# Optimization experiments

Hardware: AMD Instinct MI355X
Metric: run time of the kernel (lower is better)

The kernel has to match this reference:

```python
import jax, jax.numpy as jnp
import numpy as np

B, C, Himg, Wimg = 32, 256, 64, 64
P = 8            # partition (window) size
HEADS, DH = 8, 32
SEQ = P * P      # tokens per window = 64
SCALE = C ** (-0.5)  # note: feat_dim**-0.5, as in the source
EPS = 1e-5


def _relative_position_index(h, w):
    coords = np.stack(np.meshgrid(np.arange(h), np.arange(w), indexing='ij'))  # [2,h,w]
    cf = coords.reshape(2, -1)
    rel = cf[:, :, None] - cf[:, None, :]            # [2,hw,hw]
    rel = rel.transpose(1, 2, 0)
    rel[:, :, 0] += h - 1
    rel[:, :, 1] += w - 1
    rel[:, :, 0] *= 2 * w - 1
    return rel.sum(-1)                               # [hw,hw] int

REL_IDX = jnp.asarray(_relative_position_index(P, P).reshape(-1))  # [SEQ*SEQ]


def layernorm(x, g, b):
    mu = jnp.mean(x, -1, keepdims=True)
    var = jnp.mean(jnp.square(x - mu), -1, keepdims=True)
    return (x - mu) * jax.lax.rsqrt(var + EPS) * g + b


def setup_inputs() -> dict:
    key = jax.random.key(0)
    ks = jax.random.split(key, 12)
    d = {}
    d['x'] = jax.random.normal(ks[0], (B, C, Himg, Wimg), jnp.float32)
    d['ln1_g'] = jnp.ones((C,), jnp.float32)
    d['ln1_b'] = jnp.zeros((C,), jnp.float32)
    d['qkv_w'] = jax.random.normal(ks[1], (C, 3 * C), jnp.float32) * 0.02
    d['qkv_b'] = jnp.zeros((3 * C,), jnp.float32)
    d['merge_w'] = jax.random.normal(ks[2], (C, C), jnp.float32) * 0.02
    d['merge_b'] = jnp.zeros((C,), jnp.float32)
    d['bias_table'] = jax.random.normal(ks[3], ((2 * P - 1) * (2 * P - 1), HEADS), jnp.float32) * 0.02
    d['ln2_g'] = jnp.ones((C,), jnp.float32)
    d['ln2_b'] = jnp.zeros((C,), jnp.float32)
    d['mlp_w1'] = jax.random.normal(ks[4], (C, 4 * C), jnp.float32) * 0.02
    d['mlp_b1'] = jnp.zeros((4 * C,), jnp.float32)
    d['mlp_w2'] = jax.random.normal(ks[5], (4 * C, C), jnp.float32) * 0.02
    d['mlp_b2'] = jnp.zeros((C,), jnp.float32)
    return d


def reference(x, ln1_g, ln1_b, qkv_w, qkv_b, merge_w, merge_b, bias_table,
              ln2_g, ln2_b, mlp_w1, mlp_b1, mlp_w2, mlp_b2):
    Bn, Cn, H, W = x.shape
    hp, wp = H // P, W // P
    # window partition: [B,C,H,W] -> [B, G, P*P, C]
    xw = x.reshape(Bn, Cn, hp, P, wp, P).transpose(0, 2, 4, 3, 5, 1)
    xw = xw.reshape(Bn, hp * wp, P * P, Cn)

    # --- attention block ---
    h = layernorm(xw, ln1_g, ln1_b)
    qkv = h @ qkv_w + qkv_b                                    # [B,G,S,3C]
    q, k, v = jnp.split(qkv, 3, axis=-1)
    def heads(t):
        return t.reshape(Bn, hp * wp, SEQ, HEADS, DH).transpose(0, 1, 3, 2, 4)
    q, k, v = heads(q), heads(k) * SCALE, heads(v)             # [B,G,h,S,d]
    scores = jnp.einsum('bghid,bghjd->bghij', q, k)            # [B,G,h,S,S]
    rel_bias = bias_table[REL_IDX].reshape(SEQ, SEQ, HEADS).transpose(2, 0, 1)
    attn = jax.nn.softmax(scores + rel_bias[None, None], axis=-1)
    out = jnp.einsum('bghij,bghjd->bghid', attn, v)            # [B,G,h,S,d]
    out = out.transpose(0, 1, 3, 2, 4).reshape(Bn, hp * wp, SEQ, Cn)
    xw = xw + (out @ merge_w + merge_b)

    # --- MLP block ---
    h = layernorm(xw, ln2_g, ln2_b)
    h = jax.nn.gelu(h @ mlp_w1 + mlp_b1, approximate=False)
    xw = xw + (h @ mlp_w2 + mlp_b2)

    # window departition: [B,G,P*P,C] -> [B,C,H,W]
    y = xw.reshape(Bn, hp, wp, P, P, Cn).transpose(0, 5, 1, 3, 2, 4)
    return y.reshape(Bn, Cn, hp * P, wp * P)
```

## Files before the change

kernel.cpp:

```cpp
#include <hip/hip_runtime.h>

typedef __attribute__((ext_vector_type(8))) short short8;
typedef __attribute__((ext_vector_type(4))) short short4v;
typedef __attribute__((ext_vector_type(8))) unsigned short ushort8v;
typedef __attribute__((ext_vector_type(4))) float f32x4;
typedef __attribute__((ext_vector_type(4))) int int4v;
typedef __attribute__((ext_vector_type(4))) unsigned short ushort4v;
typedef __attribute__((ext_vector_type(2))) unsigned short ushort2v;

#define SCALE_F 0.0625f
#define EPS_F 1e-5f

__device__ __forceinline__ float bf2f(unsigned short u) {
  unsigned int i = ((unsigned int)u) << 16;
  return __builtin_bit_cast(float, i);
}
__device__ __forceinline__ unsigned short f2bf(float f) {
  unsigned int i = __builtin_bit_cast(unsigned int, f);
  i += 0x7fffu + ((i >> 16) & 1u);
  return (unsigned short)(i >> 16);
}

__device__ __forceinline__ float fast_gelu(float v) {
  float s = v * v;
  float u = v * __builtin_fmaf(s, 0.0713548163f, 1.5957691216f);
  float e = __expf(u);
  float r = __builtin_amdgcn_rcpf(e + 1.f);
  return v - v * r;
}

__device__ __forceinline__ void gload_lds16(const unsigned short* g, unsigned short* l) {
  __builtin_amdgcn_global_load_lds(
      (const __attribute__((address_space(1))) void*)g,
      (__attribute__((address_space(3))) void*)l, 16, 0, 0);
}

template<int K, int N>
__global__ void cast_wt(const float* __restrict__ src, unsigned short* __restrict__ dst) {
  int id = blockIdx.x * 256 + threadIdx.x;
  if (id >= K * N) return;
  int k = id % K, n = id / K;
  dst[id] = f2bf(src[(size_t)k * N + n]);
}

__global__ void build_relb(const float* __restrict__ table, float* __restrict__ relb) {
  int id = blockIdx.x * 256 + threadIdx.x;
  int h = id >> 12, i = (id >> 6) & 63, j = id & 63;
  int dy = (i >> 3) - (j >> 3) + 7;
  int dx = (i & 7) - (j & 7) + 7;
  relb[id] = table[(dy * 15 + dx) * 8 + h];
}

#define PLN_RS 264
__global__ __launch_bounds__(256) void part_ln1(
    const float* __restrict__ x, const float* __restrict__ g, const float* __restrict__ bb,
    unsigned short* __restrict__ h) {
  __shared__ __align__(16) unsigned short t_lds[128 * PLN_RS];
  __shared__ float ps_sum[128][2];
  __shared__ float ps_ss[128][2];
  const int tid = threadIdx.x;
  const int bid = blockIdx.x;
  const int b = bid >> 5, wr = (bid >> 2) & 7, cp = bid & 3;
  const int r0 = wr * 8;
  const int c0 = cp * 16;

  const int q = tid & 3, r = (tid >> 2) & 7, cb = tid >> 5;
  const float* xb = x + (size_t)b * 256 * 4096 + (size_t)(r0 + r) * 64 + c0 + q * 4;
#pragma unroll
  for (int it = 0; it < 16; it++) {
    int cpair = it * 8 + cb;
    const float* p0 = xb + (size_t)(2 * cpair) * 4096;
    f32x4 v0 = *(const f32x4*)p0;
    f32x4 v1 = *(const f32x4*)(p0 + 4096);
#pragma unroll
    for (int j = 0; j < 4; j++) {
      int px = r * 16 + q * 4 + j;
      ushort2v u = { f2bf(v0[j]), f2bf(v1[j]) };
      *(ushort2v*)(&t_lds[px * PLN_RS + 2 * cpair]) = u;
    }
  }
  __syncthreads();

  {
    const int p = tid & 127, half = tid >> 7;
    float sum = 0.f, ss = 0.f;
#pragma unroll
    for (int i = 0; i < 16; i++) {
      ushort8v u = *(const ushort8v*)(&t_lds[p * PLN_RS + half * 128 + i * 8]);
#pragma unroll
      for (int e = 0; e < 8; e++) { float f = bf2f(u[e]); sum += f; ss += f * f; }
    }
    ps_sum[p][half] = sum;
    ps_ss[p][half] = ss;
  }
  __syncthreads();

#pragma unroll
  for (int w = 0; w < 16; w++) {
    int id = w * 256 + tid;
    int p = id >> 5, ch = id & 31;
    float mu = (ps_sum[p][0] + ps_sum[p][1]) * (1.f / 256.f);
    float var = (ps_ss[p][0] + ps_ss[p][1]) * (1.f / 256.f) - mu * mu;
    float rs = rsqrtf(var + EPS_F);
    ushort8v u = *(const ushort8v*)(&t_lds[p * PLN_RS + ch * 8]);
    f32x4 g0 = *(const f32x4*)(g + ch * 8);
    f32x4 g1 = *(const f32x4*)(g + ch * 8 + 4);
    f32x4 b0 = *(const f32x4*)(bb + ch * 8);
    f32x4 b1 = *(const f32x4*)(bb + ch * 8 + 4);
    ushort8v o;
#pragma unroll
    for (int e = 0; e < 4; e++) {
      o[e]     = f2bf((bf2f(u[e])     - mu) * rs * g0[e] + b0[e]);
      o[e + 4] = f2bf((bf2f(u[e + 4]) - mu) * rs * g1[e] + b1[e]);
    }
    int rr = p >> 4, col = p & 15;
    size_t m = (size_t)b * 4096 + (size_t)(wr * 8 + cp * 2 + (col >> 3)) * 64 + rr * 8 + (col & 7);
    *(ushort8v*)(h + m * 256 + ch * 8) = o;
  }
}

__global__ __launch_bounds__(256) void ln2k(
    const unsigned short* __restrict__ x2, const float* __restrict__ g, const float* __restrict__ bb,
    unsigned short* __restrict__ h2) {
  int m = blockIdx.x * 4 + (threadIdx.x >> 6);
  int l = threadIdx.x & 63;
  ushort4v u = *(const ushort4v*)(x2 + (size_t)m * 256 + l * 4);
  float v[4];
  float sum = 0.f, ss = 0.f;
#pragma unroll
  for (int j = 0; j < 4; j++) { v[j] = bf2f(u[j]); sum += v[j]; ss += v[j] * v[j]; }
#pragma unroll
  for (int d = 1; d < 64; d <<= 1) {
    sum += __shfl_xor(sum, d, 64);
    ss  += __shfl_xor(ss, d, 64);
  }
  float mu = sum * (1.f / 256.f);
  float var = ss * (1.f / 256.f) - mu * mu;
  float rs = rsqrtf(var + EPS_F);
  ushort4v oh;
#pragma unroll
  for (int j = 0; j < 4; j++) {
    int c = l * 4 + j;
    oh[j] = f2bf((v[j] - mu) * rs * g[c] + bb[c]);
  }
  *(ushort4v*)(h2 + (size_t)m * 256 + l * 4) = oh;
}

enum { EPI_QKV = 0, EPI_MERGE = 1 };

template<int EPI>
__device__ __forceinline__ void gemm_body(
    unsigned short* As, unsigned short* Bs,
    const unsigned short* __restrict__ A, const unsigned short* __restrict__ Bt,
    const float* __restrict__ bias, const void* __restrict__ res,
    void* __restrict__ out, int K, int N, long m_base) {
  const int tid = threadIdx.x;
  const int l15 = tid & 15, lhi = (tid & 63) >> 4;
  const int wid = tid >> 6, wm = wid >> 1, wn = wid & 1;
  const size_t m0 = (size_t)blockIdx.x * 128;
  const int n0 = blockIdx.y * 128;
  const int row_s = tid >> 3, kc8 = (tid & 7) * 8;

  auto stage = [&](int kb, int k0) {
#pragma unroll
    for (int i = 0; i < 4; i++) {
      int row = i * 32 + row_s;
      gload_lds16(A + (m0 + row) * (size_t)K + k0 + kc8, &As[kb * 8192 + (i * 256 + tid) * 8]);
      gload_lds16(Bt + (size_t)(n0 + row) * (size_t)K + k0 + kc8, &Bs[kb * 8192 + (i * 256 + tid) * 8]);
    }
  };

  f32x4 acc[4][4];
#pragma unroll
  for (int i = 0; i < 4; i++)
#pragma unroll
    for (int j = 0; j < 4; j++) acc[i][j] = (f32x4){0.f, 0.f, 0.f, 0.f};

  stage(0, 0);
  int kb = 0;
  for (int k0 = 0; k0 < K; k0 += 64, kb ^= 1) {
    if (k0 + 64 < K) {
      stage(kb ^ 1, k0 + 64);
      asm volatile("s_waitcnt vmcnt(8)" ::: "memory");
    } else {
      asm volatile("s_waitcnt vmcnt(0)" ::: "memory");
    }
    __builtin_amdgcn_s_barrier();
#pragma unroll
    for (int ks = 0; ks < 2; ks++) {
      short8 af[4], bfr[4];
#pragma unroll
      for (int t = 0; t < 4; t++) {
        af[t]  = *(const short8*)(&As[kb * 8192 + (wm * 64 + t * 16 + l15) * 64 + ks * 32 + lhi * 8]);
        bfr[t] = *(const short8*)(&Bs[kb * 8192 + (wn * 64 + t * 16 + l15) * 64 + ks * 32 + lhi * 8]);
      }
#pragma unroll
      for (int mt = 0; mt < 4; mt++)
#pragma unroll
        for (int nt = 0; nt < 4; nt++)
          acc[mt][nt] = __builtin_amdgcn_mfma_f32_16x16x32_bf16(af[mt], bfr[nt], acc[mt][nt], 0, 0, 0);
    }
    __builtin_amdgcn_s_barrier();
  }

#pragma unroll
  for (int mt = 0; mt < 4; mt++) {
#pragma unroll
    for (int nt = 0; nt < 4; nt++) {
      const size_t gml0 = m0 + wm * 64 + mt * 16 + lhi * 4;
      const size_t gm0 = gml0 + (size_t)m_base;
      const int gn = n0 + wn * 64 + nt * 16 + l15;
      if (EPI == EPI_QKV) {
#pragma unroll
        for (int r = 0; r < 4; r++)
          ((unsigned short*)out)[(gml0 + r) * (size_t)N + gn] = f2bf(acc[mt][nt][r] + bias[gn]);
      } else {
        int bi = (int)(gm0 >> 12), gg = (int)((gm0 >> 6) & 63), s0 = (int)(gm0 & 63);
        size_t sp = (size_t)((gg >> 3) * 8 + (s0 >> 3)) * 64 + (gg & 7) * 8 + (s0 & 7);
        f32x4 xr = *(const f32x4*)(&((const float*)res)[((size_t)(bi * 256 + gn)) * 4096 + sp]);
#pragma unroll
        for (int r = 0; r < 4; r++)
          ((unsigned short*)out)[(gm0 + r) * 256 + gn] = f2bf(acc[mt][nt][r] + bias[gn] + xr[r]);
      }
    }
  }
}

#define GEMM_WRAP(name, epi)                                                          \
__global__ __launch_bounds__(256) void name(                                          \
    const unsigned short* __restrict__ A, const unsigned short* __restrict__ Bt,      \
    const float* __restrict__ bias, const void* __restrict__ res,                     \
    void* __restrict__ out, int K, int N, long m_base) {                              \
  __shared__ __align__(16) unsigned short As[2 * 128 * 64];                           \
  __shared__ __align__(16) unsigned short Bs[2 * 128 * 64];                           \
  gemm_body<epi>(As, Bs, A, Bt, bias, res, out, K, N, m_base);                        \
}
GEMM_WRAP(gemm_qkv, EPI_QKV)
GEMM_WRAP(gemm_merge, EPI_MERGE)

#define A2S 132
__global__ __launch_bounds__(256, 2) void mlp_fused(
    const unsigned short* __restrict__ h2, const unsigned short* __restrict__ w1t,
    const float* __restrict__ b1, const unsigned short* __restrict__ w2t,
    const float* __restrict__ b2, const unsigned short* __restrict__ x2,
    float* __restrict__ out) {
  __shared__ __align__(16) unsigned short Ash[64 * 256];
  __shared__ __align__(16) unsigned short A2sh[64 * A2S];
  const int tid = threadIdx.x;
  const int wid = tid >> 6, l = tid & 63, l15 = l & 15, lhi = l >> 4;
  const size_t m0 = (size_t)blockIdx.x * 64;

#pragma unroll
  for (int i = 0; i < 8; i++) {
    int uidx = i * 256 + tid;
    int row = uidx >> 5, su = uidx & 31;
    int gu = su ^ ((row & 15) << 1);
    gload_lds16(h2 + (m0 + row) * 256 + gu * 8, &Ash[uidx * 8]);
  }
  asm volatile("s_waitcnt vmcnt(0)" ::: "memory");
  __builtin_amdgcn_s_barrier();

  f32x4 oacc[4][4];
#pragma unroll
  for (int i = 0; i < 4; i++)
#pragma unroll
    for (int j = 0; j < 4; j++) oacc[i][j] = (f32x4){0.f, 0.f, 0.f, 0.f};

  for (int hs = 0; hs < 8; hs++) {
    f32x4 hacc[4][2];
#pragma unroll
    for (int i = 0; i < 4; i++) { hacc[i][0] = (f32x4){0.f,0.f,0.f,0.f}; hacc[i][1] = (f32x4){0.f,0.f,0.f,0.f}; }
    const int hc0 = hs * 128 + wid * 32;
#pragma unroll
    for (int kst = 0; kst < 8; kst++) {
      short8 af[4], bf1[2];
#pragma unroll
      for (int mt = 0; mt < 4; mt++) {
        int su = (kst * 4 + lhi) ^ ((l15 & 15) << 1);
        af[mt] = *(const short8*)(&Ash[(mt * 16 + l15) * 256 + su * 8]);
      }
#pragma unroll
      for (int nt = 0; nt < 2; nt++)
        bf1[nt] = *(const short8*)(w1t + (size_t)(hc0 + nt * 16 + l15) * 256 + kst * 32 + lhi * 8);
#pragma unroll
      for (int mt = 0; mt < 4; mt++)
#pragma unroll
        for (int nt = 0; nt < 2; nt++)
          hacc[mt][nt] = __builtin_amdgcn_mfma_f32_16x16x32_bf16(af[mt], bf1[nt], hacc[mt][nt], 0, 0, 0);
    }
    float bv0 = b1[hc0 + l15], bv1 = b1[hc0 + 16 + l15];
#pragma unroll
    for (int mt = 0; mt < 4; mt++)
#pragma unroll
      for (int nt = 0; nt < 2; nt++) {
        float bv = nt ? bv1 : bv0;
        int kh = wid * 32 + nt * 16 + l15;
#pragma unroll
        for (int rr = 0; rr < 4; rr++) {
          float v = hacc[mt][nt][rr] + bv;
          A2sh[(mt * 16 + lhi * 4 + rr) * A2S + kh] = f2bf(fast_gelu(v));
        }
      }
    __builtin_amdgcn_s_barrier();
#pragma unroll
    for (int k2 = 0; k2 < 4; k2++) {
      short8 a2[4], bf2v[4];
#pragma unroll
      for (int mt = 0; mt < 4; mt++) {
        const unsigned short* p = &A2sh[(mt * 16 + l15) * A2S + k2 * 32 + lhi * 8];
        short4v lo = *(const short4v*)p;
        short4v hi = *(const short4v*)(p + 4);
        a2[mt] = (short8){lo[0], lo[1], lo[2], lo[3], hi[0], hi[1], hi[2], hi[3]};
      }
#pragma unroll
      for (int nt = 0; nt < 4; nt++)
        bf2v[nt] = *(const short8*)(w2t + (size_t)(wid * 64 + nt * 16 + l15) * 1024 +
                                    hs * 128 + k2 * 32 + lhi * 8);
#pragma unroll
      for (int mt = 0; mt < 4; mt++)
#pragma unroll
        for (int nt = 0; nt < 4; nt++)
          oacc[mt][nt] = __builtin_amdgcn_mfma_f32_16x16x32_bf16(a2[mt], bf2v[nt], oacc[mt][nt], 0, 0, 0);
    }
    __builtin_amdgcn_s_barrier();
  }

#pragma unroll
  for (int mt = 0; mt < 4; mt++) {
#pragma unroll
    for (int nt = 0; nt < 4; nt++) {
      size_t gm0 = m0 + mt * 16 + lhi * 4;
      int gn = wid * 64 + nt * 16 + l15;
      int bi = (int)(gm0 >> 12), gg = (int)((gm0 >> 6) & 63), s0 = (int)(gm0 & 63);
      size_t sp = (size_t)((gg >> 3) * 8 + (s0 >> 3)) * 64 + (gg & 7) * 8 + (s0 & 7);
      f32x4 o4;
#pragma unroll
      for (int r = 0; r < 4; r++)
        o4[r] = oacc[mt][nt][r] + b2[gn] + bf2f(x2[(gm0 + r) * 256 + gn]);
      *(f32x4*)(&out[((size_t)(bi * 256 + gn)) * 4096 + sp]) = o4;
    }
  }
}

__global__ __launch_bounds__(64) void attn_k(
    const unsigned short* __restrict__ qkv, const float* __restrict__ relb,
    unsigned short* __restrict__ o) {
  __shared__ __align__(16) unsigned short p_lds[64 * 72];
  __shared__ __align__(16) unsigned short vt_lds[32 * 72];
  const int l = threadIdx.x;
  const int l15 = l & 15, lhi = l >> 4;
  const int w = blockIdx.x, head = blockIdx.y;
  const unsigned short* base = qkv + (size_t)w * 64 * 768 + head * 32;

  short8 aq[4], bk[4];
#pragma unroll
  for (int t = 0; t < 4; t++) {
    aq[t] = *(const short8*)(base + (t * 16 + l15) * 768 + lhi * 8);
    bk[t] = *(const short8*)(base + 256 + (t * 16 + l15) * 768 + lhi * 8);
  }
  f32x4 s[4][4];
#pragma unroll
  for (int i = 0; i < 4; i++)
#pragma unroll
    for (int j = 0; j < 4; j++) s[i][j] = (f32x4){0.f, 0.f, 0.f, 0.f};
#pragma unroll
  for (int mt = 0; mt < 4; mt++)
#pragma unroll
    for (int nt = 0; nt < 4; nt++)
      s[mt][nt] = __builtin_amdgcn_mfma_f32_16x16x32_bf16(aq[mt], bk[nt], s[mt][nt], 0, 0, 0);

  const float* rb = relb + head * 4096;
  float rsum[4][4];
#pragma unroll
  for (int mt = 0; mt < 4; mt++) {
#pragma unroll
    for (int r = 0; r < 4; r++) {
      int row = mt * 16 + lhi * 4 + r;
      float vv[4];
      float vmax = -1e30f;
#pragma unroll
      for (int nt = 0; nt < 4; nt++) {
        int col = nt * 16 + l15;
        float v = s[mt][nt][r] * SCALE_F + rb[row * 64 + col];
        vv[nt] = v;
        vmax = fmaxf(vmax, v);
      }
#pragma unroll
      for (int d = 1; d < 16; d <<= 1) vmax = fmaxf(vmax, __shfl_xor(vmax, d, 64));
      float sum = 0.f;
#pragma unroll
      for (int nt = 0; nt < 4; nt++) {
        float p = __expf(vv[nt] - vmax);
        sum += p;
        p_lds[row * 72 + nt * 16 + l15] = f2bf(p);
      }
#pragma unroll
      for (int d = 1; d < 16; d <<= 1) sum += __shfl_xor(sum, d, 64);
      rsum[mt][r] = 1.f / sum;
    }
  }

#pragma unroll
  for (int j = 0; j < 4; j++) {
    short8 vv = *(const short8*)(base + 512 + l * 768 + j * 8);
#pragma unroll
    for (int e = 0; e < 8; e++)
      vt_lds[(j * 8 + e) * 72 + l] = (unsigned short)vv[e];
  }
  __syncthreads();

  f32x4 o2[4][2];
#pragma unroll
  for (int i = 0; i < 4; i++) { o2[i][0] = (f32x4){0.f,0.f,0.f,0.f}; o2[i][1] = (f32x4){0.f,0.f,0.f,0.f}; }
#pragma unroll
  for (int ks = 0; ks < 2; ks++) {
    short8 ap[4], bv[2];
#pragma unroll
    for (int t = 0; t < 4; t++)
      ap[t] = *(const short8*)(&p_lds[(t * 16 + l15) * 72 + ks * 32 + lhi * 8]);
#pragma unroll
    for (int t = 0; t < 2; t++)
      bv[t] = *(const short8*)(&vt_lds[(t * 16 + l15) * 72 + ks * 32 + lhi * 8]);
#pragma unroll
    for (int mt = 0; mt < 4; mt++)
#pragma unroll
      for (int n2 = 0; n2 < 2; n2++)
        o2[mt][n2] = __builtin_amdgcn_mfma_f32_16x16x32_bf16(ap[mt], bv[n2], o2[mt][n2], 0, 0, 0);
  }
#pragma unroll
  for (int mt = 0; mt < 4; mt++)
#pragma unroll
    for (int n2 = 0; n2 < 2; n2++)
#pragma unroll
      for (int r = 0; r < 4; r++) {
        int row = mt * 16 + lhi * 4 + r;
        int dh = n2 * 16 + l15;
        o[((size_t)w * 64 + row) * 256 + head * 32 + dh] = f2bf(o2[mt][n2][r] * rsum[mt][r]);
      }
}

extern "C" void kernel_launch(void* const* d_in, const int* in_sizes, int n_in,
                              void* d_out, int out_size, void* d_ws, size_t ws_size,
                              hipStream_t stream) {
  (void)in_sizes; (void)n_in; (void)out_size;
  const float* x          = (const float*)d_in[0];
  const float* ln1_g      = (const float*)d_in[1];
  const float* ln1_b      = (const float*)d_in[2];
  const float* qkv_w      = (const float*)d_in[3];
  const float* qkv_b      = (const float*)d_in[4];
  const float* merge_w    = (const float*)d_in[5];
  const float* merge_b    = (const float*)d_in[6];
  const float* bias_table = (const float*)d_in[7];
  const float* ln2_g      = (const float*)d_in[8];
  const float* ln2_b      = (const float*)d_in[9];
  const float* mlp_w1     = (const float*)d_in[10];
  const float* mlp_b1     = (const float*)d_in[11];
  const float* mlp_w2     = (const float*)d_in[12];
  const float* mlp_b2     = (const float*)d_in[13];

  const size_t MB = 1024ull * 1024ull;
  char* ws = (char*)d_ws;
  unsigned short* buf0 = (unsigned short*)(ws);
  unsigned short* x2   = (unsigned short*)(ws + 64 * MB);
  unsigned short* wqkv = (unsigned short*)(ws + 128 * MB);
  unsigned short* wmrg = wqkv + 768 * 256;
  unsigned short* w1t  = wmrg + 256 * 256;
  unsigned short* w2t  = w1t + 1024 * 256;
  float* relb          = (float*)(w2t + 256 * 1024);
  unsigned short* Cbuf = (unsigned short*)(ws + 130 * MB);

  size_t avail = ws_size > 130 * MB ? ws_size - 130 * MB : 0;
  int wc = 64;
  {
    const int cands[3] = {512, 256, 128};
    for (int i = 0; i < 3; i++)
      if ((size_t)cands[i] * 64 * 768 * 2 <= avail) { wc = cands[i]; break; }
  }

  cast_wt<256, 768><<<768, 256, 0, stream>>>(qkv_w, wqkv);
  cast_wt<256, 256><<<256, 256, 0, stream>>>(merge_w, wmrg);
  cast_wt<256, 1024><<<1024, 256, 0, stream>>>(mlp_w1, w1t);
  cast_wt<1024, 256><<<1024, 256, 0, stream>>>(mlp_w2, w2t);
  build_relb<<<128, 256, 0, stream>>>(bias_table, relb);

  part_ln1<<<1024, 256, 0, stream>>>(x, ln1_g, ln1_b, buf0);

  for (int w0 = 0; w0 < 2048; w0 += wc) {
    gemm_qkv<<<dim3(wc * 64 / 128, 6), 256, 0, stream>>>(
        buf0 + (size_t)w0 * 64 * 256, wqkv, qkv_b, nullptr, Cbuf, 256, 768, 0);
    attn_k<<<dim3(wc, 8), 64, 0, stream>>>(Cbuf, relb, buf0 + (size_t)w0 * 64 * 256);
  }

  gemm_merge<<<dim3(1024, 2), 256, 0, stream>>>(
      buf0, wmrg, merge_b, x, x2, 256, 256, 0);

  ln2k<<<32768, 256, 0, stream>>>(x2, ln2_g, ln2_b, buf0);

  mlp_fused<<<2048, 256, 0, stream>>>(buf0, w1t, mlp_b1, w2t, mlp_b2, x2, (float*)d_out);
}
```

Baseline: 741.6 us.

## Software-pipeline fused MLP: double-buffer GELU tile and overlap GEMM1/GEMM2 stages

The fused MLP kernel now double-buffers the GELU intermediate in shared memory. Each iteration prefetches the next slice's W1 fragments into registers, runs GEMM2 on the current slice, then computes GEMM1 and GELU for the next slice into the other buffer. This removes one barrier per iteration and hides the W1 global-load latency behind GEMM2. It also raises wave priority around the MFMA blocks. The cost is more LDS (a second A2 buffer) and more registers for the 16 prefetched W1 fragments, which may hurt occupancy under launch_bounds(256,2).

```diff
diff --git a/kernel.cpp b/kernel.cpp
--- a/kernel.cpp
+++ b/kernel.cpp
@@ -245,7 +245,7 @@
     const float* __restrict__ b2, const unsigned short* __restrict__ x2,
     float* __restrict__ out) {
   __shared__ __align__(16) unsigned short Ash[64 * 256];
-  __shared__ __align__(16) unsigned short A2sh[64 * A2S];
+  __shared__ __align__(16) unsigned short A2sh[2][64 * A2S];
   const int tid = threadIdx.x;
   const int wid = tid >> 6, l = tid & 63, l15 = l & 15, lhi = l >> 4;
   const size_t m0 = (size_t)blockIdx.x * 64;
@@ -266,28 +266,41 @@
 #pragma unroll
     for (int j = 0; j < 4; j++) oacc[i][j] = (f32x4){0.f, 0.f, 0.f, 0.f};
 
-  for (int hs = 0; hs < 8; hs++) {
-    f32x4 hacc[4][2];
-#pragma unroll
-    for (int i = 0; i < 4; i++) { hacc[i][0] = (f32x4){0.f,0.f,0.f,0.f}; hacc[i][1] = (f32x4){0.f,0.f,0.f,0.f}; }
-    const int hc0 = hs * 128 + wid * 32;
+  auto gemm1_mfma = [&](short8 w1f[8][2], f32x4 hacc[4][2]) {
+#pragma unroll
+    for (int i = 0; i < 4; i++) {
+      hacc[i][0] = (f32x4){0.f, 0.f, 0.f, 0.f};
+      hacc[i][1] = (f32x4){0.f, 0.f, 0.f, 0.f};
+    }
+    __builtin_amdgcn_s_setprio(1);
 #pragma unroll
     for (int kst = 0; kst < 8; kst++) {
-      short8 af[4], bf1[2];
+      short8 af[4];
 #pragma unroll
       for (int mt = 0; mt < 4; mt++) {
         int su = (kst * 4 + lhi) ^ ((l15 & 15) << 1);
         af[mt] = *(const short8*)(&Ash[(mt * 16 + l15) * 256 + su * 8]);
       }
 #pragma unroll
+      for (int mt = 0; mt < 4; mt++)
+#pragma unroll
+        for (int nt = 0; nt < 2; nt++)
+          hacc[mt][nt] = __builtin_amdgcn_mfma_f32_16x16x32_bf16(af[mt], w1f[kst][nt], hacc[mt][nt], 0, 0, 0);
+    }
+    __builtin_amdgcn_s_setprio(0);
+  };
+
+  auto load_w1 = [&](int hs, short8 w1f[8][2]) {
+    const int hc0 = hs * 128 + wid * 32;
+#pragma unroll
+    for (int kst = 0; kst < 8; kst++)
+#pragma unroll
       for (int nt = 0; nt < 2; nt++)
-        bf1[nt] = *(const short8*)(w1t + (size_t)(hc0 + nt * 16 + l15) * 256 + kst * 32 + lhi * 8);
-#pragma unroll
-      for (int mt = 0; mt < 4; mt++)
-#pragma unroll
-        for (int nt = 0; nt < 2; nt++)
-          hacc[mt][nt] = __builtin_amdgcn_mfma_f32_16x16x32_bf16(af[mt], bf1[nt], hacc[mt][nt], 0, 0, 0);
-    }
+        w1f[kst][nt] = *(const short8*)(w1t + (size_t)(hc0 + nt * 16 + l15) * 256 + kst * 32 + lhi * 8);
+  };
+
+  auto gelu_store = [&](int hs, int buf, f32x4 hacc[4][2]) {
+    const int hc0 = hs * 128 + wid * 32;
     float bv0 = b1[hc0 + l15], bv1 = b1[hc0 + 16 + l15];
 #pragma unroll
     for (int mt = 0; mt < 4; mt++)
@@ -298,16 +311,18 @@
 #pragma unroll
         for (int rr = 0; rr < 4; rr++) {
           float v = hacc[mt][nt][rr] + bv;
-          A2sh[(mt * 16 + lhi * 4 + rr) * A2S + kh] = f2bf(fast_gelu(v));
+          A2sh[buf][(mt * 16 + lhi * 4 + rr) * A2S + kh] = f2bf(fast_gelu(v));
         }
       }
-    __builtin_amdgcn_s_barrier();
+  };
+
+  auto gemm2 = [&](int hs, int buf) {
 #pragma unroll
     for (int k2 = 0; k2 < 4; k2++) {
       short8 a2[4], bf2v[4];
 #pragma unroll
       for (int mt = 0; mt < 4; mt++) {
-        const unsigned short* p = &A2sh[(mt * 16 + l15) * A2S + k2 * 32 + lhi * 8];
+        const unsigned short* p = &A2sh[buf][(mt * 16 + l15) * A2S + k2 * 32 + lhi * 8];
         short4v lo = *(const short4v*)p;
         short4v hi = *(const short4v*)(p + 4);
         a2[mt] = (short8){lo[0], lo[1], lo[2], lo[3], hi[0], hi[1], hi[2], hi[3]};
@@ -316,11 +331,36 @@
       for (int nt = 0; nt < 4; nt++)
         bf2v[nt] = *(const short8*)(w2t + (size_t)(wid * 64 + nt * 16 + l15) * 1024 +
                                     hs * 128 + k2 * 32 + lhi * 8);
+      __builtin_amdgcn_s_setprio(1);
 #pragma unroll
       for (int mt = 0; mt < 4; mt++)
 #pragma unroll
         for (int nt = 0; nt < 4; nt++)
           oacc[mt][nt] = __builtin_amdgcn_mfma_f32_16x16x32_bf16(a2[mt], bf2v[nt], oacc[mt][nt], 0, 0, 0);
+      __builtin_amdgcn_s_setprio(0);
+    }
+  };
+
+  {
+    short8 w1f[8][2];
+    f32x4 hacc[4][2];
+    load_w1(0, w1f);
+    gemm1_mfma(w1f, hacc);
+    gelu_store(0, 0, hacc);
+  }
+  __builtin_amdgcn_s_barrier();
+
+  for (int s = 0; s < 8; s++) {
+    int buf = s & 1;
+    if (s < 7) {
+      short8 w1f[8][2];
+      f32x4 hacc[4][2];
+      load_w1(s + 1, w1f);
+      gemm2(s, buf);
+      gemm1_mfma(w1f, hacc);
+      gelu_store(s + 1, buf ^ 1, hacc);
+    } else {
+      gemm2(s, buf);
     }
     __builtin_amdgcn_s_barrier();
   }
```

After: 799.4 us. 1.08x slower.
